# Optimization experiments

Measured on AMD Instinct MI355X. Metric: run time of the kernel, lower is better.

## Reference

```python
import jax, jax.numpy as jnp
import numpy as np

# module constants (from init_kwargs)
CS, NV, ED = 8, 4, 32          # codebook_size, num_variables, embedding_dim
VIEWS, D, KSZ = 3, 16, 3        # num_input_channels, depth, kernel_size
HW = 14                         # 7 * scale (scale=2)
CSP = 8                         # spatial of conv_shape after three valid 3x3 convs: 14->12->10->8
KSTATES = CS ** NV              # 4096 combinatorial discrete states


def _elu(x):
    return jnp.where(x > 0, x, jnp.expm1(x))


def _conv_t(x, w, b):
    # PyTorch ConvTranspose2d(stride=1, padding=0); w: (Cin, Cout, k, k)
    wf = jnp.flip(w, (2, 3)).transpose(1, 0, 2, 3)  # -> (Cout, Cin, k, k)
    p = w.shape[2] - 1
    y = jax.lax.conv_general_dilated(x, wf, (1, 1), [(p, p), (p, p)],
                                     dimension_numbers=('NCHW', 'OIHW', 'NCHW'))
    return y + b[None, :, None, None]


def setup_inputs() -> dict:
    key = jax.random.key(0)
    ks = jax.random.split(key, 10)
    rn = lambda k, shape, s=1.0: jax.random.normal(k, shape, jnp.float32) * s
    return {
        'x': rn(ks[0], (64, VIEWS, HW, HW)),
        'latent_embedding': rn(ks[1], (NV, CS, ED)),
        'lin_w': rn(ks[2], (VIEWS, ED * NV, 4 * D * CSP * CSP), 0.05),
        'lin_b': rn(ks[3], (VIEWS, 4 * D * CSP * CSP), 0.05),
        'w1': rn(ks[4], (VIEWS, 4 * D, 2 * D, KSZ, KSZ), 0.05),
        'b1': rn(ks[5], (VIEWS, 2 * D), 0.05),
        'w2': rn(ks[6], (VIEWS, 2 * D, D, KSZ, KSZ), 0.05),
        'b2': rn(ks[7], (VIEWS, D), 0.05),
        'w3': rn(ks[8], (VIEWS, D, 1, KSZ, KSZ), 0.05),
        'b3': rn(ks[9], (VIEWS, 1), 0.05),
    }


def reference(x, latent_embedding, lin_w, lin_b, w1, b1, w2, b2, w3, b3):
    # all combinations of codebook indices (itertools.product order): [K, NV]
    all_idcs = jnp.stack(
        jnp.meshgrid(*([jnp.arange(CS)] * NV), indexing='ij'), -1).reshape(-1, NV)
    # gather: z[k, v, :] = latent_embedding[v, all_idcs[k, v], :]
    z = latent_embedding[jnp.arange(NV)[None, :], all_idcs]       # [K, NV, ED]
    zf = z.reshape(KSTATES, NV * ED)                              # 'b n d -> b (n d)'

    def decode(lw, lb, W1, B1, W2, B2, W3, B3):
        h = (zf @ lw + lb).reshape(KSTATES, 4 * D, CSP, CSP)
        h = _elu(_conv_t(h, W1, B1))
        h = _elu(_conv_t(h, W2, B2))
        h = _conv_t(h, W3, B3)
        return h[:, 0]                                            # [K, HW, HW]

    m = jax.vmap(decode)(lin_w, lin_b, w1, b1, w2, b2, w3, b3)    # [views, K, HW, HW]
    m = jnp.transpose(m, (1, 0, 2, 3))                            # [K, views, HW, HW]

    # obs_logits = -0.5 * sum_{h,w} (m[None] - x[:, None])**2, computed without
    # materializing the [B, K, views, HW, HW] broadcast tensor
    m2 = jnp.sum(m * m, axis=(-2, -1))                            # [K, views]
    x2 = jnp.sum(x * x, axis=(-2, -1))                            # [B, views]
    cross = jnp.einsum('kvhw,bvhw->bkv', m, x)                    # [B, K, views]
    return -0.5 * (m2[None] + x2[:, None] - 2.0 * cross)          # [B, K, views]
```

## Files before the change

### kernel.cpp

```cpp
#include <hip/hip_runtime.h>
#include <cstddef>


typedef __attribute__((ext_vector_type(4))) float f32x4;
typedef _Float16 half8v __attribute__((ext_vector_type(8)));
typedef _Float16 half4v __attribute__((ext_vector_type(4)));
typedef _Float16 half2v __attribute__((ext_vector_type(2)));

static __device__ __forceinline__ float elu(float s) {
    float e = __expf(s) - 1.0f;
    return s > 0.f ? s : e;
}
static __device__ __forceinline__ float dot2acc(int hpair, int wpair, float acc) {
#if __has_builtin(__builtin_amdgcn_fdot2)
    return __builtin_amdgcn_fdot2(__builtin_bit_cast(half2v, hpair),
                                  __builtin_bit_cast(half2v, wpair), acc, false);
#else
    half2v h = __builtin_bit_cast(half2v, hpair);
    half2v w = __builtin_bit_cast(half2v, wpair);
    acc = fmaf((float)h.x, (float)w.x, acc);
    return fmaf((float)h.y, (float)w.y, acc);
#endif
}
static __device__ __forceinline__ int sh2addr(int c, int r) {
    return c * 392 + r * 24 + (((r >> 2) & 3) << 3);
}

__global__ __launch_bounds__(320) void prep_kernel(const float* __restrict__ x,
                                                   const float* __restrict__ le,
                                                   const float* __restrict__ lin_w,
                                                   const float* __restrict__ lin_b,
                                                   const float* __restrict__ w1,
                                                   const float* __restrict__ b1,
                                                   const float* __restrict__ w2,
                                                   float* __restrict__ Qa,
                                                   float* __restrict__ Qb,
                                                   float* __restrict__ x2,
                                                   short* __restrict__ xB,
                                                   short* __restrict__ Wf) {
    int bid = blockIdx.x;
    int t = threadIdx.x;
    if (bid >= 198) {
        int pid = bid - 198;
        int v = pid % 3, part = pid / 3;
        if (part < 4) {
            int nb = part;
            short* xBv = xB + v * 14336 + nb * 3584;
            for (int idx = t; idx < 3584; idx += 320) {
                int j = idx & 7, lane = (idx >> 3) & 63, s = idx >> 9;
                int px = s * 32 + ((lane >> 4) << 3) + j;
                int b  = nb * 16 + (lane & 15);
                float val = (px < 196) ? x[(b * 3 + v) * 196 + px] : 0.f;
                _Float16 h = (_Float16)val;
                xBv[idx] = __builtin_bit_cast(short, h);
            }
        } else if (part == 4) {
            int w = t >> 6, lane = t & 63;
            for (int b = w; b < 64; b += 5) {
                const float* xp = x + (b * 3 + v) * 196;
                float s = 0.f;
                for (int px = lane; px < 196; px += 64) s = fmaf(xp[px], xp[px], s);
#pragma unroll
                for (int off = 32; off; off >>= 1) s += __shfl_down(s, off, 64);
                if (lane == 0) x2[v * 64 + b] = s;
            }
        } else if (t < 64) {
            int lane = t;
            const float* w2v = w2 + v * 32 * 16 * 9;
            int co = lane & 15;
            int cibase = (lane >> 4) * 8;
#pragma unroll
            for (int tap = 0; tap < 9; ++tap)
#pragma unroll
                for (int j = 0; j < 8; ++j) {
                    _Float16 h = (_Float16)w2v[((cibase + j) * 16 + co) * 9 + tap];
                    Wf[(((v * 9 + tap) * 64 + lane) << 3) + j] = __builtin_bit_cast(short, h);
                }
        }
        return;
    }
    __shared__ float sPt[64 * 144];
    __shared__ float sW[16 * 32 * 9];
    int row = bid % 33;
    int v   = (bid / 33) % 3;
    int z   = bid / 99;

    float pj[16];
    if (t < 256) {
        if (row < 32) {
            int vp = row >> 3;
            const float* base0 = lin_w + (size_t)v * 524288 + (size_t)vp * 131072 + t * 16;
            const float* lep = le + row * 32;
            f32x4 a0 = {0,0,0,0}, a1 = {0,0,0,0}, a2 = {0,0,0,0}, a3 = {0,0,0,0};
            for (int e = 0; e < 32; ++e) {
                float lv = lep[e];
                const float4* bp = (const float4*)(base0 + e * 4096);
                float4 b0 = bp[0], b1v_ = bp[1], b2v_ = bp[2], b3v_ = bp[3];
                a0[0] = fmaf(lv, b0.x, a0[0]);  a0[1] = fmaf(lv, b0.y, a0[1]);
                a0[2] = fmaf(lv, b0.z, a0[2]);  a0[3] = fmaf(lv, b0.w, a0[3]);
                a1[0] = fmaf(lv, b1v_.x, a1[0]); a1[1] = fmaf(lv, b1v_.y, a1[1]);
                a1[2] = fmaf(lv, b1v_.z, a1[2]); a1[3] = fmaf(lv, b1v_.w, a1[3]);
                a2[0] = fmaf(lv, b2v_.x, a2[0]); a2[1] = fmaf(lv, b2v_.y, a2[1]);
                a2[2] = fmaf(lv, b2v_.z, a2[2]); a2[3] = fmaf(lv, b2v_.w, a2[3]);
                a3[0] = fmaf(lv, b3v_.x, a3[0]); a3[1] = fmaf(lv, b3v_.y, a3[1]);
                a3[2] = fmaf(lv, b3v_.z, a3[2]); a3[3] = fmaf(lv, b3v_.w, a3[3]);
            }
#pragma unroll
            for (int j = 0; j < 4; ++j) {
                pj[j] = a0[j]; pj[4 + j] = a1[j]; pj[8 + j] = a2[j]; pj[12 + j] = a3[j];
            }
        } else {
            const float4* bp = (const float4*)(lin_b + v * 4096 + t * 16);
#pragma unroll
            for (int j = 0; j < 4; ++j) {
                float4 b = bp[j];
                pj[4 * j] = b.x; pj[4 * j + 1] = b.y; pj[4 * j + 2] = b.z; pj[4 * j + 3] = b.w;
            }
        }
    }
    float4* zp = (float4*)sPt;
    for (int i = t; i < 2304; i += 320) zp[i] = float4{0.f, 0.f, 0.f, 0.f};
    __syncthreads();
    if (t < 256) {
        int ci = t >> 2;
#pragma unroll
        for (int j = 0; j < 16; ++j) {
            int r = (t & 3) * 16 + j;
            int y = r >> 3, xx = r & 7;
            sPt[ci * 144 + (xx + 2) * 12 + (y + 2)] = pj[j];
        }
    }
    const float* w1v = w1 + (size_t)v * 18432;
    int co = t / 10, ox = t % 10;
    float acc[10];
#pragma unroll
    for (int i = 0; i < 10; ++i) acc[i] = 0.f;

    for (int c0 = z * 2; c0 < z * 2 + 2; ++c0) {
        __syncthreads();
        const float4* wsrc = (const float4*)(w1v + c0 * 4608);
        for (int i = t; i < 1152; i += 320) ((float4*)sW)[i] = wsrc[i];
        __syncthreads();
#pragma unroll 2
        for (int ci = 0; ci < 16; ++ci) {
            const float* xp = sPt + (c0 * 16 + ci) * 144;
            const float* wp = sW + (ci * 32 + co) * 9;
            float wv[9];
#pragma unroll
            for (int j = 0; j < 9; ++j) wv[j] = wp[j];
#pragma unroll
            for (int b = 0; b < 3; ++b) {
                const float* colp = xp + (ox + 2 - b) * 12;
                float4 c0v = *(const float4*)(colp);
                float4 c1v = *(const float4*)(colp + 4);
                float4 c2v = *(const float4*)(colp + 8);
                float cv[12] = {c0v.x, c0v.y, c0v.z, c0v.w,
                                c1v.x, c1v.y, c1v.z, c1v.w,
                                c2v.x, c2v.y, c2v.z, c2v.w};
#pragma unroll
                for (int a = 0; a < 3; ++a) {
                    float wgt = wv[a * 3 + b];
#pragma unroll
                    for (int oy = 0; oy < 10; ++oy)
                        acc[oy] = fmaf(cv[oy + 2 - a], wgt, acc[oy]);
                }
            }
        }
    }
    float bb = (z == 0 && row == 32) ? b1[v * 32 + co] : 0.f;
    float* dst = (z == 0 ? Qa : Qb) + (size_t)v * 105600 + row * 3200;
#pragma unroll
    for (int oy = 0; oy < 10; ++oy)
        dst[(ox * 10 + oy) * 32 + co] = acc[oy] + bb;
}

__global__ __launch_bounds__(256) void pair_kernel(const float* __restrict__ Qa,
                                                   const float* __restrict__ Qb,
                                                   float* __restrict__ Q01,
                                                   float* __restrict__ Q23b) {
    int p = blockIdx.x;
    int half = blockIdx.y;
    int v = blockIdx.z;
    const float4* basea = (const float4*)(Qa + (size_t)v * 105600);
    const float4* baseb = (const float4*)(Qb + (size_t)v * 105600);
    if (half == 0) {
        const float4* ra = basea + (p >> 3) * 800;
        const float4* rb = baseb + (p >> 3) * 800;
        const float4* rc = basea + (8 + (p & 7)) * 800;
        const float4* rd = baseb + (8 + (p & 7)) * 800;
        float4* dst = (float4*)(Q01 + (size_t)v * 204800 + p * 3200);
        for (int i = threadIdx.x; i < 800; i += 256) {
            float4 a = ra[i], b = rb[i], c = rc[i], d = rd[i];
            dst[i] = float4{a.x + b.x + c.x + d.x, a.y + b.y + c.y + d.y,
                            a.z + b.z + c.z + d.z, a.w + b.w + c.w + d.w};
        }
    } else {
        const float4* ra = basea + (16 + (p >> 3)) * 800;
        const float4* rb = baseb + (16 + (p >> 3)) * 800;
        const float4* rc = basea + (24 + (p & 7)) * 800;
        const float4* rd = baseb + (24 + (p & 7)) * 800;
        const float4* re = basea + 32 * 800;
        const float4* rf = baseb + 32 * 800;
        float4* dst = (float4*)(Q23b + (size_t)v * 204800 + p * 3200);
        for (int i = threadIdx.x; i < 800; i += 256) {
            float4 a = ra[i], b = rb[i], c = rc[i], d = rd[i], e = re[i], f = rf[i];
            dst[i] = float4{a.x + b.x + c.x + d.x + e.x + f.x,
                            a.y + b.y + c.y + d.y + e.y + f.y,
                            a.z + b.z + c.z + d.z + e.z + f.z,
                            a.w + b.w + c.w + d.w + e.w + f.w};
        }
    }
}

__global__ __launch_bounds__(256) void fused_kernel(const float* __restrict__ Q01,
                                                    const float* __restrict__ Q23b,
                                                    const short* __restrict__ Wf,
                                                    const float* __restrict__ b2,
                                                    const float* __restrict__ w3,
                                                                const float* __restrict__ b3,
                                                    short* __restrict__ Mh,
                                                    float* __restrict__ m2g) {
    __shared__ alignas(16) short sH1[196 * 40];
    __shared__ alignas(16) short sH2[6280];
    __shared__ int sW3p[72];
    __shared__ float sM2[2];
    int k0 = blockIdx.x * 2;
    int v = blockIdx.y;
    int t = threadIdx.x;
    int lane = t & 63;
    int g = lane >> 4;

    half8v bfrag[9];
#pragma unroll
    for (int tap = 0; tap < 9; ++tap)
        bfrag[tap] = *(const half8v*)(const void*)(Wf + (((v * 9 + tap) * 64 + lane) << 3));
    float bias2 = b2[v * 16 + (lane & 15)];

    if (t < 2) sM2[t] = 0.f;
    for (int pix = t; pix < 196; pix += 256) {
        int c = pix / 14, r = pix % 14;
        if (c < 2 || c >= 12 || r < 2 || r >= 12) {
            int4* z = (int4*)(sH1 + pix * 40);
            z[0] = int4{0,0,0,0}; z[1] = int4{0,0,0,0};
            z[2] = int4{0,0,0,0}; z[3] = int4{0,0,0,0};
        }
    }
    {
        int c = t >> 4, r = t & 15;
        if (c < 2 || c >= 14 || r < 2 || r >= 14) {
            int4* z = (int4*)(sH2 + sh2addr(c, r));
            z[0] = int4{0,0,0,0}; z[1] = int4{0,0,0,0};
        }
    }
    if (t < 72) {
        int tap = t / 8, j = t % 8;
        half2v p = {(_Float16)w3[v * 144 + (2 * j) * 9 + tap],
                    (_Float16)w3[v * 144 + (2 * j + 1) * 9 + tap]};
        sW3p[t] = __builtin_bit_cast(int, p);
    }

    const float4* qa = (const float4*)(Q01 + ((size_t)v * 64 + (k0 >> 6)) * 3200);
    float4 ra[4];

#pragma unroll
    for (int s = 0; s < 2; ++s) {
        int k = k0 + s;
        {
            const float4* qb = (const float4*)(Q23b + ((size_t)v * 64 + (k & 63)) * 3200);
            int ci4 = (t & 7) * 4;
            int pix = t >> 3;
            int cx = pix / 10, ry = pix % 10;
#pragma unroll
            for (int j = 0; j < 4; ++j) {
                int i = t + j * 256;
                if (i < 800) {
                    if (s == 0) ra[j] = qa[i];
                    float4 a = ra[j];
                    float4 b = qb[i];
                    half4v o = {(_Float16)elu(a.x + b.x), (_Float16)elu(a.y + b.y),
                                (_Float16)elu(a.z + b.z), (_Float16)elu(a.w + b.w)};
                    *(half4v*)(void*)(sH1 + ((cx + 2) * 14 + (ry + 2)) * 40 + ci4) = o;
                }
                cx += 3; ry += 2;
                if (ry >= 10) { ry -= 10; ++cx; }
            }
        }
        __syncthreads();
        {
            int w = t >> 6;
            for (int tile = w; tile < 9; tile += 4) {
                int m = tile * 16 + (lane & 15);
                int cx2 = m / 12, ry2 = m % 12;
                const short* basemin = sH1 + (cx2 * 14 + ry2) * 40 + g * 8;
                f32x4 acc0 = {bias2, bias2, bias2, bias2};
                f32x4 acc1 = {0.f, 0.f, 0.f, 0.f};
#pragma unroll
                for (int a = 0; a < 3; ++a)
#pragma unroll
                    for (int b = 0; b < 3; ++b) {
                        half8v af = *(const half8v*)(const void*)(basemin + ((2 - b) * 14 + (2 - a)) * 40);
                        int idx = a * 3 + b;
                        if (idx & 1)
                            acc1 = __builtin_amdgcn_mfma_f32_16x16x32_f16(af, bfrag[idx], acc1, 0, 0, 0);
                        else
                            acc0 = __builtin_amdgcn_mfma_f32_16x16x32_f16(af, bfrag[idx], acc0, 0, 0, 0);
                    }
                int p0 = tile * 16 + g * 4;
                int cxp = p0 / 12, ryp = p0 % 12;
                int co = lane & 15;
#pragma unroll
                for (int r = 0; r < 4; ++r) {
                    _Float16 h = (_Float16)elu(acc0[r] + acc1[r]);
                    sH2[sh2addr(cxp + 2, ryp + 2) + co] = __builtin_bit_cast(short, h);
                    ++ryp; if (ryp == 12) { ryp = 0; ++cxp; }
                }
            }
        }
        __syncthreads();
        {
            float mval = 0.f;
            if (t < 196) {
                float bias3 = b3[v];
                int ry3 = t / 14, cx3 = t % 14;
                float a0 = bias3, a1 = 0.f, a2 = 0.f, a3 = 0.f;
#pragma unroll
                for (int a = 0; a < 3; ++a)
#pragma unroll
                    for (int b = 0; b < 3; ++b) {
                        const short* base = sH2 + sh2addr(cx3 + 2 - b, ry3 + 2 - a);
                        int4 lo = *(const int4*)(const void*)(base);
                        int4 hi = *(const int4*)(const void*)(base + 8);
                        const int* wp = sW3p + (a * 3 + b) * 8;
                        a0 = dot2acc(lo.x, wp[0], a0);
                        a1 = dot2acc(lo.y, wp[1], a1);
                        a2 = dot2acc(lo.z, wp[2], a2);
                        a3 = dot2acc(lo.w, wp[3], a3);
                        a0 = dot2acc(hi.x, wp[4], a0);
                        a1 = dot2acc(hi.y, wp[5], a1);
                        a2 = dot2acc(hi.z, wp[6], a2);
                        a3 = dot2acc(hi.w, wp[7], a3);
                    }
                mval = (a0 + a1) + (a2 + a3);
            }
            if (t < 224) {
                _Float16 h = (_Float16)mval;
                Mh[((size_t)v * 4096 + k) * 224 + t] = __builtin_bit_cast(short, h);
            }
            float sq = mval * mval;
#pragma unroll
            for (int off = 32; off; off >>= 1) sq += __shfl_down(sq, off, 64);
            if (lane == 0) atomicAdd(&sM2[s], sq);
        }
    }
    __syncthreads();
    if (t < 2) m2g[(size_t)v * 4096 + k0 + t] = sM2[t];
}

__global__ __launch_bounds__(256) void gemm_final_kernel(const short* __restrict__ Mh,
                                                         const short* __restrict__ xB,
                                                         const float* __restrict__ m2g,
                                                         const float* __restrict__ x2g,
                                                         float* __restrict__ out) {
    __shared__ float sC[3 * 64 * 17];
    __shared__ float sM2t[48];
    int t = threadIdx.x, lane = t & 63, nb = t >> 6;
    int k0 = blockIdx.x * 16;
    if (t < 48) {
        int v = t % 3, kk = t / 3;
        sM2t[kk * 3 + v] = m2g[(size_t)v * 4096 + k0 + kk];
    }
    int mrow = lane & 15;
    int g = lane >> 4;
#pragma unroll
    for (int v = 0; v < 3; ++v) {
        f32x4 acc = {0.f, 0.f, 0.f, 0.f};
        const short* abase = Mh + ((size_t)v * 4096 + k0 + mrow) * 224 + g * 8;
        const short* bbase = xB + (((v * 4 + nb) * 7) * 64 + lane) * 8;
#pragma unroll
        for (int s = 0; s < 7; ++s) {
            half8v af = *(const half8v*)(const void*)(abase + s * 32);
            half8v bf = *(const half8v*)(const void*)(bbase + s * 512);
            acc = __builtin_amdgcn_mfma_f32_16x16x32_f16(af, bf, acc, 0, 0, 0);
        }
        int b = nb * 16 + mrow;
#pragma unroll
        for (int r = 0; r < 4; ++r)
            sC[(v * 64 + b) * 17 + g * 4 + r] = acc[r];
    }
    __syncthreads();
    int b = t >> 2, q = t & 3;
    float x2v0 = x2g[b], x2v1 = x2g[64 + b], x2v2 = x2g[128 + b];
    float buf[12];
#pragma unroll
    for (int i = 0; i < 4; ++i) {
        int kk = q * 4 + i;
        buf[i * 3 + 0] = sC[(0 * 64 + b) * 17 + kk] - 0.5f * (sM2t[kk * 3 + 0] + x2v0);
        buf[i * 3 + 1] = sC[(1 * 64 + b) * 17 + kk] - 0.5f * (sM2t[kk * 3 + 1] + x2v1);
        buf[i * 3 + 2] = sC[(2 * 64 + b) * 17 + kk] - 0.5f * (sM2t[kk * 3 + 2] + x2v2);
    }
    float* dst = out + ((size_t)b * 4096 + k0) * 3 + q * 12;
    *(float4*)(dst)     = float4{buf[0], buf[1], buf[2],  buf[3]};
    *(float4*)(dst + 4) = float4{buf[4], buf[5], buf[6],  buf[7]};
    *(float4*)(dst + 8) = float4{buf[8], buf[9], buf[10], buf[11]};
}

extern "C" void kernel_launch(void* const* d_in, const int* in_sizes, int n_in,
                              void* d_out, int out_size, void* d_ws, size_t ws_size,
                              hipStream_t stream) {
    const float* x     = (const float*)d_in[0];
    const float* le    = (const float*)d_in[1];
    const float* lin_w = (const float*)d_in[2];
    const float* lin_b = (const float*)d_in[3];
    const float* w1    = (const float*)d_in[4];
    const float* b1    = (const float*)d_in[5];
    const float* w2    = (const float*)d_in[6];
    const float* b2    = (const float*)d_in[7];
    const float* w3    = (const float*)d_in[8];
    const float* b3    = (const float*)d_in[9];
    float* out = (float*)d_out;

    float* ws = (float*)d_ws;
    float* x2g  = ws;
    short* xB   = (short*)(ws + 192);
    short* Wf   = (short*)(ws + 21760);
    float* Qa   = ws + 28736;
    float* Qb   = ws + 345536;
    float* Q01  = ws + 662336;
    float* Q23b = ws + 1276736;
    short* Mh   = (short*)(ws + 1891136);
    float* m2g  = ws + 3267392;

    prep_kernel<<<216, 320, 0, stream>>>(x, le, lin_w, lin_b, w1, b1, w2,
                                         Qa, Qb, x2g, xB, Wf);
    pair_kernel<<<dim3(64, 2, 3), 256, 0, stream>>>(Qa, Qb, Q01, Q23b);
    fused_kernel<<<dim3(2048, 3), 256, 0, stream>>>(Q01, Q23b, Wf, b2, w3, b3, Mh, m2g);
    gemm_final_kernel<<<256, 256, 0, stream>>>(Mh, xB, m2g, x2g, out);
}
```

Baseline: 175.0 us.

## Fuse decoder and final GEMM, processing 16 states per block

```diff
diff --git a/kernel.cpp b/kernel.cpp
--- a/kernel.cpp
+++ b/kernel.cpp
@@ -212,31 +212,35 @@
     }
 }
 
-__global__ __launch_bounds__(256) void fused_kernel(const float* __restrict__ Q01,
-                                                    const float* __restrict__ Q23b,
-                                                    const short* __restrict__ Wf,
-                                                    const float* __restrict__ b2,
-                                                    const float* __restrict__ w3,
-                                                                const float* __restrict__ b3,
-                                                    short* __restrict__ Mh,
-                                                    float* __restrict__ m2g) {
+__global__ __launch_bounds__(256) void fusedgemm_kernel(const float* __restrict__ Q01,
+                                                        const float* __restrict__ Q23b,
+                                                        const short* __restrict__ Wf,
+                                                        const float* __restrict__ b2,
+                                                        const float* __restrict__ w3,
+                                                        const float* __restrict__ b3,
+                                                        const short* __restrict__ xB,
+                                                        const float* __restrict__ x2g,
+                                                        float* __restrict__ out) {
     __shared__ alignas(16) short sH1[196 * 40];
     __shared__ alignas(16) short sH2[6280];
+    __shared__ alignas(16) short sM[16 * 224];
     __shared__ int sW3p[72];
-    __shared__ float sM2[2];
-    int k0 = blockIdx.x * 2;
+    __shared__ float sM2[16];
+    int k0 = blockIdx.x * 16;
     int v = blockIdx.y;
     int t = threadIdx.x;
     int lane = t & 63;
     int g = lane >> 4;
+    int w = t >> 6;
 
     half8v bfrag[9];
 #pragma unroll
     for (int tap = 0; tap < 9; ++tap)
         bfrag[tap] = *(const half8v*)(const void*)(Wf + (((v * 9 + tap) * 64 + lane) << 3));
     float bias2 = b2[v * 16 + (lane & 15)];
-
-    if (t < 2) sM2[t] = 0.f;
+    float bias3 = b3[v];
+
+    if (t < 16) sM2[t] = 0.f;
     for (int pix = t; pix < 196; pix += 256) {
         int c = pix / 14, r = pix % 14;
         if (c < 2 || c >= 12 || r < 2 || r >= 12) {
@@ -259,39 +263,69 @@
         sW3p[t] = __builtin_bit_cast(int, p);
     }
 
+    int st1[4]; bool v1[4];
+    {
+        int ci4 = (t & 7) * 4;
+#pragma unroll
+        for (int j = 0; j < 4; ++j) {
+            int i = t + j * 256;
+            v1[j] = (i < 800);
+            int pix = i >> 3;
+            int cx = pix / 10, ry = pix % 10;
+            st1[j] = ((cx + 2) * 14 + (ry + 2)) * 40 + ci4;
+        }
+    }
+    int ntile = 0; int bmoff[3]; int soff[3][4];
+    for (int tile = w; tile < 9; tile += 4) {
+        int m = tile * 16 + (lane & 15);
+        int cx2 = m / 12, ry2 = m % 12;
+        bmoff[ntile] = (cx2 * 14 + ry2) * 40 + g * 8;
+        int p0 = tile * 16 + g * 4;
+        int cxp = p0 / 12, ryp = p0 % 12;
+        int co = lane & 15;
+#pragma unroll
+        for (int r = 0; r < 4; ++r) {
+            soff[ntile][r] = sh2addr(cxp + 2, ryp + 2) + co;
+            ++ryp; if (ryp == 12) { ryp = 0; ++cxp; }
+        }
+        ++ntile;
+    }
+    int off3[9];
+    {
+        int ry3 = (t < 196) ? t / 14 : 0;
+        int cx3 = (t < 196) ? t % 14 : 0;
+#pragma unroll
+        for (int a = 0; a < 3; ++a)
+#pragma unroll
+            for (int b = 0; b < 3; ++b)
+                off3[a * 3 + b] = sh2addr(cx3 + 2 - b, ry3 + 2 - a);
+    }
+
     const float4* qa = (const float4*)(Q01 + ((size_t)v * 64 + (k0 >> 6)) * 3200);
     float4 ra[4];
-
-#pragma unroll
-    for (int s = 0; s < 2; ++s) {
-        int k = k0 + s;
+    int kb = k0 & 63;
+
+    for (int s = 0; s < 16; ++s) {
         {
-            const float4* qb = (const float4*)(Q23b + ((size_t)v * 64 + (k & 63)) * 3200);
-            int ci4 = (t & 7) * 4;
-            int pix = t >> 3;
-            int cx = pix / 10, ry = pix % 10;
+            const float4* qb = (const float4*)(Q23b + ((size_t)v * 64 + (kb + s)) * 3200);
 #pragma unroll
             for (int j = 0; j < 4; ++j) {
-                int i = t + j * 256;
-                if (i < 800) {
+                if (v1[j]) {
+                    int i = t + j * 256;
                     if (s == 0) ra[j] = qa[i];
                     float4 a = ra[j];
                     float4 b = qb[i];
                     half4v o = {(_Float16)elu(a.x + b.x), (_Float16)elu(a.y + b.y),
                                 (_Float16)elu(a.z + b.z), (_Float16)elu(a.w + b.w)};
-                    *(half4v*)(void*)(sH1 + ((cx + 2) * 14 + (ry + 2)) * 40 + ci4) = o;
+                    *(half4v*)(void*)(sH1 + st1[j]) = o;
                 }
-                cx += 3; ry += 2;
-                if (ry >= 10) { ry -= 10; ++cx; }
             }
         }
         __syncthreads();
-        {
-            int w = t >> 6;
-            for (int tile = w; tile < 9; tile += 4) {
-                int m = tile * 16 + (lane & 15);
-                int cx2 = m / 12, ry2 = m % 12;
-                const short* basemin = sH1 + (cx2 * 14 + ry2) * 40 + g * 8;
+#pragma unroll
+        for (int it = 0; it < 3; ++it) {
+            if (it < ntile) {
+                const short* basemin = sH1 + bmoff[it];
                 f32x4 acc0 = {bias2, bias2, bias2, bias2};
                 f32x4 acc1 = {0.f, 0.f, 0.f, 0.f};
 #pragma unroll
@@ -305,14 +339,10 @@
                         else
                             acc0 = __builtin_amdgcn_mfma_f32_16x16x32_f16(af, bfrag[idx], acc0, 0, 0, 0);
                     }
-                int p0 = tile * 16 + g * 4;
-                int cxp = p0 / 12, ryp = p0 % 12;
-                int co = lane & 15;
 #pragma unroll
                 for (int r = 0; r < 4; ++r) {
                     _Float16 h = (_Float16)elu(acc0[r] + acc1[r]);
-                    sH2[sh2addr(cxp + 2, ryp + 2) + co] = __builtin_bit_cast(short, h);
-                    ++ryp; if (ryp == 12) { ryp = 0; ++cxp; }
+                    sH2[soff[it][r]] = __builtin_bit_cast(short, h);
                 }
             }
         }
@@ -320,31 +350,27 @@
         {
             float mval = 0.f;
             if (t < 196) {
-                float bias3 = b3[v];
-                int ry3 = t / 14, cx3 = t % 14;
                 float a0 = bias3, a1 = 0.f, a2 = 0.f, a3 = 0.f;
 #pragma unroll
-                for (int a = 0; a < 3; ++a)
-#pragma unroll
-                    for (int b = 0; b < 3; ++b) {
-                        const short* base = sH2 + sh2addr(cx3 + 2 - b, ry3 + 2 - a);
-                        int4 lo = *(const int4*)(const void*)(base);
-                        int4 hi = *(const int4*)(const void*)(base + 8);
-                        const int* wp = sW3p + (a * 3 + b) * 8;
-                        a0 = dot2acc(lo.x, wp[0], a0);
-                        a1 = dot2acc(lo.y, wp[1], a1);
-                        a2 = dot2acc(lo.z, wp[2], a2);
-                        a3 = dot2acc(lo.w, wp[3], a3);
-                        a0 = dot2acc(hi.x, wp[4], a0);
-                        a1 = dot2acc(hi.y, wp[5], a1);
-                        a2 = dot2acc(hi.z, wp[6], a2);
-                        a3 = dot2acc(hi.w, wp[7], a3);
-                    }
+                for (int tap = 0; tap < 9; ++tap) {
+                    const short* base = sH2 + off3[tap];
+                    int4 lo = *(const int4*)(const void*)(base);
+                    int4 hi = *(const int4*)(const void*)(base + 8);
+                    const int* wp = sW3p + tap * 8;
+                    a0 = dot2acc(lo.x, wp[0], a0);
+                    a1 = dot2acc(lo.y, wp[1], a1);
+                    a2 = dot2acc(lo.z, wp[2], a2);
+                    a3 = dot2acc(lo.w, wp[3], a3);
+                    a0 = dot2acc(hi.x, wp[4], a0);
+                    a1 = dot2acc(hi.y, wp[5], a1);
+                    a2 = dot2acc(hi.z, wp[6], a2);
+                    a3 = dot2acc(hi.w, wp[7], a3);
+                }
                 mval = (a0 + a1) + (a2 + a3);
             }
             if (t < 224) {
                 _Float16 h = (_Float16)mval;
-                Mh[((size_t)v * 4096 + k) * 224 + t] = __builtin_bit_cast(short, h);
+                sM[s * 224 + t] = __builtin_bit_cast(short, h);
             }
             float sq = mval * mval;
 #pragma unroll
@@ -353,55 +379,26 @@
         }
     }
     __syncthreads();
-    if (t < 2) m2g[(size_t)v * 4096 + k0 + t] = sM2[t];
-}
-
-__global__ __launch_bounds__(256) void gemm_final_kernel(const short* __restrict__ Mh,
-                                                         const short* __restrict__ xB,
-                                                         const float* __restrict__ m2g,
-                                                         const float* __restrict__ x2g,
-                                                         float* __restrict__ out) {
-    __shared__ float sC[3 * 64 * 17];
-    __shared__ float sM2t[48];
-    int t = threadIdx.x, lane = t & 63, nb = t >> 6;
-    int k0 = blockIdx.x * 16;
-    if (t < 48) {
-        int v = t % 3, kk = t / 3;
-        sM2t[kk * 3 + v] = m2g[(size_t)v * 4096 + k0 + kk];
-    }
-    int mrow = lane & 15;
-    int g = lane >> 4;
-#pragma unroll
-    for (int v = 0; v < 3; ++v) {
+
+    {
         f32x4 acc = {0.f, 0.f, 0.f, 0.f};
-        const short* abase = Mh + ((size_t)v * 4096 + k0 + mrow) * 224 + g * 8;
-        const short* bbase = xB + (((v * 4 + nb) * 7) * 64 + lane) * 8;
-#pragma unroll
-        for (int s = 0; s < 7; ++s) {
-            half8v af = *(const half8v*)(const void*)(abase + s * 32);
-            half8v bf = *(const half8v*)(const void*)(bbase + s * 512);
+        const short* abase = sM + (lane & 15) * 224 + g * 8;
+        const short* bbase = xB + (((v * 4 + w) * 7) * 64 + lane) * 8;
+#pragma unroll
+        for (int s7 = 0; s7 < 7; ++s7) {
+            half8v af = *(const half8v*)(const void*)(abase + s7 * 32);
+            half8v bf = *(const half8v*)(const void*)(bbase + s7 * 512);
             acc = __builtin_amdgcn_mfma_f32_16x16x32_f16(af, bf, acc, 0, 0, 0);
         }
-        int b = nb * 16 + mrow;
-#pragma unroll
-        for (int r = 0; r < 4; ++r)
-            sC[(v * 64 + b) * 17 + g * 4 + r] = acc[r];
-    }
-    __syncthreads();
-    int b = t >> 2, q = t & 3;
-    float x2v0 = x2g[b], x2v1 = x2g[64 + b], x2v2 = x2g[128 + b];
-    float buf[12];
-#pragma unroll
-    for (int i = 0; i < 4; ++i) {
-        int kk = q * 4 + i;
-        buf[i * 3 + 0] = sC[(0 * 64 + b) * 17 + kk] - 0.5f * (sM2t[kk * 3 + 0] + x2v0);
-        buf[i * 3 + 1] = sC[(1 * 64 + b) * 17 + kk] - 0.5f * (sM2t[kk * 3 + 1] + x2v1);
-        buf[i * 3 + 2] = sC[(2 * 64 + b) * 17 + kk] - 0.5f * (sM2t[kk * 3 + 2] + x2v2);
-    }
-    float* dst = out + ((size_t)b * 4096 + k0) * 3 + q * 12;
-    *(float4*)(dst)     = float4{buf[0], buf[1], buf[2],  buf[3]};
-    *(float4*)(dst + 4) = float4{buf[4], buf[5], buf[6],  buf[7]};
-    *(float4*)(dst + 8) = float4{buf[8], buf[9], buf[10], buf[11]};
+        int b = w * 16 + (lane & 15);
+        float x2v = x2g[v * 64 + b];
+        size_t obase = ((size_t)b * 4096 + k0) * 3 + v;
+#pragma unroll
+        for (int r = 0; r < 4; ++r) {
+            int kk = g * 4 + r;
+            out[obase + (size_t)kk * 3] = acc[r] - 0.5f * (sM2[kk] + x2v);
+        }
+    }
 }
 
 extern "C" void kernel_launch(void* const* d_in, const int* in_sizes, int n_in,
@@ -427,12 +424,10 @@
     float* Qb   = ws + 345536;
     float* Q01  = ws + 662336;
     float* Q23b = ws + 1276736;
-    short* Mh   = (short*)(ws + 1891136);
-    float* m2g  = ws + 3267392;
 
     prep_kernel<<<216, 320, 0, stream>>>(x, le, lin_w, lin_b, w1, b1, w2,
                                          Qa, Qb, x2g, xB, Wf);
     pair_kernel<<<dim3(64, 2, 3), 256, 0, stream>>>(Qa, Qb, Q01, Q23b);
-    fused_kernel<<<dim3(2048, 3), 256, 0, stream>>>(Q01, Q23b, Wf, b2, w3, b3, Mh, m2g);
-    gemm_final_kernel<<<256, 256, 0, stream>>>(Mh, xB, m2g, x2g, out);
-}
+    fusedgemm_kernel<<<dim3(256, 3), 256, 0, stream>>>(Q01, Q23b, Wf, b2, w3, b3,
+                                                       xB, x2g, out);
+}
```

Result: no change. 175.0 us (-0.0%).
